# Performance work log

Hardware: AMD Instinct MI355X
Metric: run time of the kernel (lower is better)

Reference implementation:

```python
import jax, jax.numpy as jnp
import numpy as np

B, N = 4, 128
INPUT_SIZE, Z_SIZE = 512, 256
D_TENSOR, N_HEADS, SEQ_LEN = 64, 8, 64
D = D_TENSOR * N_HEADS * SEQ_LEN  # 32768


def setup_inputs() -> dict:
    key = jax.random.key(0)
    ks = jax.random.split(key, 10)
    s = lambda fan_in: 1.0 / np.sqrt(fan_in)
    return {
        "x": jax.random.normal(ks[0], (B, N, INPUT_SIZE), dtype=jnp.float32),
        "z": jax.random.normal(ks[1], (B, N, Z_SIZE), dtype=jnp.float32),
        "Wq": jax.random.uniform(ks[2], (Z_SIZE, D), jnp.float32, -s(Z_SIZE), s(Z_SIZE)),
        "bq": jax.random.uniform(ks[3], (D,), jnp.float32, -s(Z_SIZE), s(Z_SIZE)),
        "Wk": jax.random.uniform(ks[4], (INPUT_SIZE, D), jnp.float32, -s(INPUT_SIZE), s(INPUT_SIZE)),
        "bk": jax.random.uniform(ks[5], (D,), jnp.float32, -s(INPUT_SIZE), s(INPUT_SIZE)),
        "Wv": jax.random.uniform(ks[6], (INPUT_SIZE, D), jnp.float32, -s(INPUT_SIZE), s(INPUT_SIZE)),
        "bv": jax.random.uniform(ks[7], (D,), jnp.float32, -s(INPUT_SIZE), s(INPUT_SIZE)),
        "Wo": jax.random.uniform(ks[8], (D, INPUT_SIZE), jnp.float32, -s(D), s(D)),
        "bo": jax.random.uniform(ks[9], (INPUT_SIZE,), jnp.float32, -s(D), s(D)),
    }


def reference(x, z, Wq, bq, Wk, bk, Wv, bv, Wo, bo):
    # Q, K, V: [B, N, heads, seq_len, d_tensor]
    Q = (z @ Wq + bq).reshape(B, N, N_HEADS, SEQ_LEN, D_TENSOR)
    K = (x @ Wk + bk).reshape(B, N, N_HEADS, SEQ_LEN, D_TENSOR)
    V = (x @ Wv + bv).reshape(B, N, N_HEADS, SEQ_LEN, D_TENSOR)
    scores = jnp.einsum("bnhqd,bnhkd->bnhqk", Q, K) / np.sqrt(D_TENSOR).astype(np.float32)
    attn = jax.nn.softmax(scores, axis=-1)
    out = jnp.einsum("bnhqk,bnhkd->bnhqd", attn, V).reshape(B, N, D)
    return out @ Wo + bo
```

## Files before the change

### kernel.cpp

```cpp
#include <hip/hip_runtime.h>
#include <stdint.h>


typedef __attribute__((ext_vector_type(8))) short short8;
typedef __attribute__((ext_vector_type(4))) float floatx4;

__device__ __forceinline__ unsigned short f2bf(float f) {
  union { float f; unsigned int u; } v; v.f = f;
  unsigned int u = v.u + 0x7FFFu + ((v.u >> 16) & 1u);
  return (unsigned short)(u >> 16);
}

#define MFMA16(a, b, c) __builtin_amdgcn_mfma_f32_16x16x32_bf16((a), (b), (c), 0, 0, 0)

#define STAGE_TILE(SRC, LD, LDSARR)                                            \
  do {                                                                         \
    _Pragma("unroll") for (int i_ = 0; i_ < 4; ++i_) {                         \
      int e_ = tid + (i_ << 8);                                                \
      int r_ = e_ >> 3;                                                        \
      int c_ = (e_ & 7) ^ (r_ & 7);                                            \
      __builtin_amdgcn_global_load_lds(                                        \
          (const __attribute__((address_space(1))) unsigned int*)((SRC) +      \
              (size_t)r_ * (LD) + (c_ << 3)),                                  \
          (__attribute__((address_space(3))) unsigned int*)(&(LDSARR)[e_ << 3]),\
          16, 0, 0);                                                           \
    }                                                                          \
  } while (0)

#define FRAG(LDSARR, ROW, KS)                                                  \
  (*(const short8*)(&(LDSARR)[(((ROW) << 6)) +                                 \
      ((((((KS) << 2) + quad)) ^ ((ROW) & 7)) << 3)]))

__device__ __forceinline__ void transpose_body(const float* __restrict__ W,
                                               unsigned short* __restrict__ WT,
                                               int Kd, int Nd) {
  __shared__ __align__(16) float S[64 * 72];
  __shared__ __align__(16) unsigned short T[64 * 72];
  const int tid = threadIdx.x;
  const int n0 = blockIdx.x * 64, k0 = blockIdx.y * 64;
#pragma unroll
  for (int i = 0; i < 4; ++i) {
    int e = tid + (i << 8);
    int r = e >> 4, c = (e & 15) << 2;
    float4 w = *(const float4*)(W + (size_t)(k0 + r) * Nd + n0 + c);
    *(float4*)(&S[r * 72 + c]) = w;
  }
  __syncthreads();
  {
    const int n = tid & 63, kh = tid >> 6;
    float v[16];
#pragma unroll
    for (int j = 0; j < 16; ++j) v[j] = S[(kh * 16 + j) * 72 + n];
    uint4 p0, p1;
    p0.x = f2bf(v[0])  | ((unsigned)f2bf(v[1])  << 16);
    p0.y = f2bf(v[2])  | ((unsigned)f2bf(v[3])  << 16);
    p0.z = f2bf(v[4])  | ((unsigned)f2bf(v[5])  << 16);
    p0.w = f2bf(v[6])  | ((unsigned)f2bf(v[7])  << 16);
    p1.x = f2bf(v[8])  | ((unsigned)f2bf(v[9])  << 16);
    p1.y = f2bf(v[10]) | ((unsigned)f2bf(v[11]) << 16);
    p1.z = f2bf(v[12]) | ((unsigned)f2bf(v[13]) << 16);
    p1.w = f2bf(v[14]) | ((unsigned)f2bf(v[15]) << 16);
    *(uint4*)(&T[n * 72 + kh * 16])     = p0;
    *(uint4*)(&T[n * 72 + kh * 16 + 8]) = p1;
  }
  __syncthreads();
#pragma unroll
  for (int i = 0; i < 2; ++i) {
    int e = tid + (i << 8);
    int n = e >> 3, kc = e & 7;
    uint4 vv = *(const uint4*)(&T[n * 72 + kc * 8]);
    *(uint4*)(WT + (size_t)(n0 + n) * Kd + k0 + kc * 8) = vv;
  }
}

__global__ __launch_bounds__(256) void transpose_qkv(const float* __restrict__ Wq,
                                                     const float* __restrict__ Wk,
                                                     const float* __restrict__ Wv,
                                                     unsigned short* __restrict__ WqT,
                                                     unsigned short* __restrict__ WkT,
                                                     unsigned short* __restrict__ WvT,
                                                     const float* __restrict__ x,
                                                     const float* __restrict__ z,
                                                     unsigned short* __restrict__ xb,
                                                     unsigned short* __restrict__ zb) {
  const int zsel = blockIdx.z;
  if (zsel == 0) {
    if (blockIdx.y >= 4) return;
    transpose_body(Wq, WqT, 256, 32768);
  } else if (zsel == 1) {
    transpose_body(Wk, WkT, 512, 32768);
  } else if (zsel == 2) {
    transpose_body(Wv, WvT, 512, 32768);
  } else {
    if (blockIdx.y != 0 || blockIdx.x >= 192) return;
    int idx = (blockIdx.x * 256 + threadIdx.x) * 8;
    const float* src;
    unsigned short* dst;
    if (idx < 262144) { src = x + idx; dst = xb + idx; }
    else              { src = z + (idx - 262144); dst = zb + (idx - 262144); }
    float4 f0 = *(const float4*)src;
    float4 f1 = *(const float4*)(src + 4);
    uint4 p;
    p.x = f2bf(f0.x) | ((unsigned)f2bf(f0.y) << 16);
    p.y = f2bf(f0.z) | ((unsigned)f2bf(f0.w) << 16);
    p.z = f2bf(f1.x) | ((unsigned)f2bf(f1.y) << 16);
    p.w = f2bf(f1.z) | ((unsigned)f2bf(f1.w) << 16);
    *(uint4*)dst = p;
  }
}

__global__ __launch_bounds__(256) void transpose_wo(const float* __restrict__ W,
                                                    unsigned short* __restrict__ WT) {
  transpose_body(W, WT, 32768, 512);
}

__global__ __launch_bounds__(256) void gemm_qkv(const unsigned short* __restrict__ xb,
                                                const unsigned short* __restrict__ zb,
                                                const unsigned short* __restrict__ WqT,
                                                const unsigned short* __restrict__ WkT,
                                                const unsigned short* __restrict__ WvT,
                                                const float* __restrict__ bq,
                                                const float* __restrict__ bk,
                                                const float* __restrict__ bv,
                                                unsigned short* __restrict__ Qb,
                                                unsigned short* __restrict__ Kb,
                                                unsigned short* __restrict__ Vb) {
  __shared__ __align__(16) unsigned short As[128 * 64];
  __shared__ __align__(16) unsigned short Bs[128 * 64];
  const int tid = threadIdx.x;
  const int zsel = blockIdx.z;
  const unsigned short* A;
  const unsigned short* BT;
  const float* bias;
  unsigned short* C;
  int Ka;
  if (zsel == 0)      { A = zb; BT = WqT; bias = bq; C = Qb; Ka = 256; }
  else if (zsel == 1) { A = xb; BT = WkT; bias = bk; C = Kb; Ka = 512; }
  else                { A = xb; BT = WvT; bias = bv; C = Vb; Ka = 512; }
  const int lane = tid & 63, wid = tid >> 6;
  const int quad = lane >> 4, l15 = lane & 15;
  const int wm = wid >> 1, wn = wid & 1;
  const int m0 = blockIdx.y * 128, n0 = blockIdx.x * 128;
  floatx4 acc[4][4] = {};
  for (int k0 = 0; k0 < Ka; k0 += 64) {
    STAGE_TILE(A + (size_t)m0 * Ka + k0, Ka, As);
    STAGE_TILE(BT + (size_t)n0 * Ka + k0, Ka, Bs);
    __syncthreads();
#pragma unroll
    for (int ks = 0; ks < 2; ++ks) {
      short8 aF[4], bF[4];
#pragma unroll
      for (int mi = 0; mi < 4; ++mi) aF[mi] = FRAG(As, wm * 64 + mi * 16 + l15, ks);
#pragma unroll
      for (int ni = 0; ni < 4; ++ni) bF[ni] = FRAG(Bs, wn * 64 + ni * 16 + l15, ks);
#pragma unroll
      for (int mi = 0; mi < 4; ++mi)
#pragma unroll
        for (int ni = 0; ni < 4; ++ni)
          acc[mi][ni] = MFMA16(aF[mi], bF[ni], acc[mi][ni]);
    }
    __syncthreads();
  }
#pragma unroll
  for (int ni = 0; ni < 4; ++ni) {
    int col = n0 + wn * 64 + ni * 16 + l15;
    float bv2 = bias[col];
#pragma unroll
    for (int mi = 0; mi < 4; ++mi) {
      int row = m0 + wm * 64 + mi * 16 + (quad << 2);
#pragma unroll
      for (int r = 0; r < 4; ++r)
        C[(size_t)(row + r) * 32768 + col] = f2bf(acc[mi][ni][r] + bv2);
    }
  }
}

__global__ __launch_bounds__(256) void attn64(const unsigned short* __restrict__ Qb,
                                              const unsigned short* __restrict__ Kb,
                                              const unsigned short* __restrict__ Vb,
                                              unsigned short* __restrict__ Ob) {
  __shared__ __align__(16) unsigned short Qs[64 * 72];
  __shared__ __align__(16) unsigned short Ks[64 * 72];
  __shared__ __align__(16) unsigned short VT[64 * 72];
  __shared__ __align__(16) unsigned short Ps[64 * 72];
  const int tid = threadIdx.x;
  const int bn = blockIdx.x >> 3, h = blockIdx.x & 7;
  const size_t base = (size_t)bn * 32768 + (size_t)h * 4096;
  const unsigned short* q = Qb + base;
  const unsigned short* k = Kb + base;
  const unsigned short* v = Vb + base;
#pragma unroll
  for (int i = 0; i < 2; ++i) {
    int e = tid + (i << 8);
    int r = e >> 3, dblk = e & 7;
    *(uint4*)(&Qs[r * 72 + dblk * 8]) = *(const uint4*)(q + r * 64 + dblk * 8);
    *(uint4*)(&Ks[r * 72 + dblk * 8]) = *(const uint4*)(k + r * 64 + dblk * 8);
    uint4 vv = *(const uint4*)(v + r * 64 + dblk * 8);
    const unsigned short* pv = (const unsigned short*)&vv;
#pragma unroll
    for (int j = 0; j < 8; ++j)
      VT[(dblk * 8 + j) * 72 + r] = pv[j];
  }
  __syncthreads();
  const int lane = tid & 63, wid = tid >> 6;
  const int quad = lane >> 4, l15 = lane & 15;
  const int qs = wid << 4;
  short8 aq0 = *(const short8*)(&Qs[(qs + l15) * 72 + quad * 8]);
  short8 aq1 = *(const short8*)(&Qs[(qs + l15) * 72 + 32 + quad * 8]);
  floatx4 s[4] = {};
#pragma unroll
  for (int ni = 0; ni < 4; ++ni) {
    short8 b0 = *(const short8*)(&Ks[(ni * 16 + l15) * 72 + quad * 8]);
    short8 b1 = *(const short8*)(&Ks[(ni * 16 + l15) * 72 + 32 + quad * 8]);
    s[ni] = MFMA16(aq0, b0, s[ni]);
    s[ni] = MFMA16(aq1, b1, s[ni]);
  }
#pragma unroll
  for (int r = 0; r < 4; ++r) {
    float e0 = s[0][r] * 0.125f, e1 = s[1][r] * 0.125f;
    float e2 = s[2][r] * 0.125f, e3 = s[3][r] * 0.125f;
    float m = fmaxf(fmaxf(e0, e1), fmaxf(e2, e3));
    m = fmaxf(m, __shfl_xor(m, 1));
    m = fmaxf(m, __shfl_xor(m, 2));
    m = fmaxf(m, __shfl_xor(m, 4));
    m = fmaxf(m, __shfl_xor(m, 8));
    float x0 = __expf(e0 - m), x1 = __expf(e1 - m);
    float x2 = __expf(e2 - m), x3 = __expf(e3 - m);
    float t = x0 + x1 + x2 + x3;
    t += __shfl_xor(t, 1); t += __shfl_xor(t, 2);
    t += __shfl_xor(t, 4); t += __shfl_xor(t, 8);
    float inv = __builtin_amdgcn_rcpf(t);
    int row = qs + (quad << 2) + r;
    Ps[row * 72 +      l15] = f2bf(x0 * inv);
    Ps[row * 72 + 16 + l15] = f2bf(x1 * inv);
    Ps[row * 72 + 32 + l15] = f2bf(x2 * inv);
    Ps[row * 72 + 48 + l15] = f2bf(x3 * inv);
  }
  __syncthreads();
  short8 ap0 = *(const short8*)(&Ps[(qs + l15) * 72 + quad * 8]);
  short8 ap1 = *(const short8*)(&Ps[(qs + l15) * 72 + 32 + quad * 8]);
  floatx4 o[4] = {};
#pragma unroll
  for (int ni = 0; ni < 4; ++ni) {
    short8 b0 = *(const short8*)(&VT[(ni * 16 + l15) * 72 + quad * 8]);
    short8 b1 = *(const short8*)(&VT[(ni * 16 + l15) * 72 + 32 + quad * 8]);
    o[ni] = MFMA16(ap0, b0, o[ni]);
    o[ni] = MFMA16(ap1, b1, o[ni]);
  }
  unsigned short* outp = Ob + base;
#pragma unroll
  for (int ni = 0; ni < 4; ++ni)
#pragma unroll
    for (int r = 0; r < 4; ++r)
      outp[(qs + (quad << 2) + r) * 64 + ni * 16 + l15] = f2bf(o[ni][r]);
}

__global__ __launch_bounds__(256) void gemm_out(const unsigned short* __restrict__ A,
                                                const unsigned short* __restrict__ BT,
                                                const float* __restrict__ bias,
                                                float* __restrict__ C) {
  __shared__ __align__(16) unsigned short As[128 * 64];
  __shared__ __align__(16) unsigned short Bs[128 * 64];
  const int tid = threadIdx.x;
  const int lane = tid & 63, wid = tid >> 6;
  const int quad = lane >> 4, l15 = lane & 15;
  const int wm = wid >> 1, wn = wid & 1;
  const int m0 = blockIdx.y * 128, n0 = blockIdx.x * 128;
  const int kbase = blockIdx.z * 1024;
  floatx4 acc[4][4] = {};
  for (int k0 = kbase; k0 < kbase + 1024; k0 += 64) {
    STAGE_TILE(A + (size_t)m0 * 32768 + k0, 32768, As);
    STAGE_TILE(BT + (size_t)n0 * 32768 + k0, 32768, Bs);
    __syncthreads();
#pragma unroll
    for (int ks = 0; ks < 2; ++ks) {
      short8 aF[4], bF[4];
#pragma unroll
      for (int mi = 0; mi < 4; ++mi) aF[mi] = FRAG(As, wm * 64 + mi * 16 + l15, ks);
#pragma unroll
      for (int ni = 0; ni < 4; ++ni) bF[ni] = FRAG(Bs, wn * 64 + ni * 16 + l15, ks);
#pragma unroll
      for (int mi = 0; mi < 4; ++mi)
#pragma unroll
        for (int ni = 0; ni < 4; ++ni)
          acc[mi][ni] = MFMA16(aF[mi], bF[ni], acc[mi][ni]);
    }
    __syncthreads();
  }
#pragma unroll
  for (int ni = 0; ni < 4; ++ni) {
    int col = n0 + wn * 64 + ni * 16 + l15;
    float bv = (blockIdx.z == 0) ? bias[col] : 0.0f;
#pragma unroll
    for (int mi = 0; mi < 4; ++mi) {
      int row = m0 + wm * 64 + mi * 16 + (quad << 2);
#pragma unroll
      for (int r = 0; r < 4; ++r)
        atomicAdd(&C[(size_t)(row + r) * 512 + col], acc[mi][ni][r] + bv);
    }
  }
}

extern "C" void kernel_launch(void* const* d_in, const int* in_sizes, int n_in,
                              void* d_out, int out_size, void* d_ws, size_t ws_size,
                              hipStream_t stream) {
  const float* x  = (const float*)d_in[0];
  const float* z  = (const float*)d_in[1];
  const float* Wq = (const float*)d_in[2];
  const float* bq = (const float*)d_in[3];
  const float* Wk = (const float*)d_in[4];
  const float* bk = (const float*)d_in[5];
  const float* Wv = (const float*)d_in[6];
  const float* bv = (const float*)d_in[7];
  const float* Wo = (const float*)d_in[8];
  const float* bo = (const float*)d_in[9];
  float* out = (float*)d_out;
  char* ws = (char*)d_ws;

  unsigned short* WqT = (unsigned short*)(ws + 0);
  unsigned short* WkT = (unsigned short*)(ws + 16777216);
  unsigned short* WvT = (unsigned short*)(ws + 50331648);
  unsigned short* Qb  = (unsigned short*)(ws + 83886080);
  unsigned short* Kb  = (unsigned short*)(ws + 117440512);
  unsigned short* Vb  = (unsigned short*)(ws + 150994944);
  unsigned short* Ob  = (unsigned short*)(ws + 0);
  unsigned short* WoT = (unsigned short*)(ws + 50331648);

  unsigned short* xb = (unsigned short*)d_out;
  unsigned short* zb = (unsigned short*)((char*)d_out + 524288);

  transpose_qkv<<<dim3(512, 8, 4), 256, 0, stream>>>(Wq, Wk, Wv, WqT, WkT, WvT,
                                                     x, z, xb, zb);

  gemm_qkv<<<dim3(256, 4, 3), 256, 0, stream>>>(xb, zb, WqT, WkT, WvT,
                                                bq, bk, bv, Qb, Kb, Vb);

  transpose_wo<<<dim3(8, 512), 256, 0, stream>>>(Wo, WoT);

  attn64<<<dim3(4096), 256, 0, stream>>>(Qb, Kb, Vb, Ob);

  hipMemsetAsync(d_out, 0, (size_t)out_size * sizeof(float), stream);
  gemm_out<<<dim3(4, 4, 32), 256, 0, stream>>>(Ob, WoT, bo, out);
}
```

Baseline: 384.3 us.

## Widen QKV GEMM tile to 128x256 and loop transposes over column strips

The QKV projection GEMM now computes a 128x256 output tile per block, with twice the B staging and an 8-wide accumulator array per warp, so each A tile is reused across more columns and fewer blocks are launched. The weight transpose kernels now process eight 64-column sub-tiles per block in a loop, which cuts the grid size by 8x, and the x/z conversion indexing is remapped to fit the smaller grid. The aim is less redundant A-tile traffic and lower block scheduling overhead. In exchange the GEMM uses more registers and LDS per block, which may lower occupancy, and the transposes have less parallelism per launch (transpose_wo drops to 512 blocks).

```diff
diff --git a/kernel.cpp b/kernel.cpp
--- a/kernel.cpp
+++ b/kernel.cpp
@@ -13,9 +13,9 @@
 
 #define MFMA16(a, b, c) __builtin_amdgcn_mfma_f32_16x16x32_bf16((a), (b), (c), 0, 0, 0)
 
-#define STAGE_TILE(SRC, LD, LDSARR)                                            \
+#define STAGE_ROWS(SRC, LD, LDSARR, NIT)                                       \
   do {                                                                         \
-    _Pragma("unroll") for (int i_ = 0; i_ < 4; ++i_) {                         \
+    _Pragma("unroll") for (int i_ = 0; i_ < (NIT); ++i_) {                     \
       int e_ = tid + (i_ << 8);                                                \
       int r_ = e_ >> 3;                                                        \
       int c_ = (e_ & 7) ^ (r_ & 7);                                            \
@@ -31,45 +31,49 @@
   (*(const short8*)(&(LDSARR)[(((ROW) << 6)) +                                 \
       ((((((KS) << 2) + quad)) ^ ((ROW) & 7)) << 3)]))
 
-__device__ __forceinline__ void transpose_body(const float* __restrict__ W,
-                                               unsigned short* __restrict__ WT,
-                                               int Kd, int Nd) {
+__device__ __forceinline__ void transpose_strip(const float* __restrict__ W,
+                                                unsigned short* __restrict__ WT,
+                                                int Kd, int Nd) {
   __shared__ __align__(16) float S[64 * 72];
   __shared__ __align__(16) unsigned short T[64 * 72];
   const int tid = threadIdx.x;
-  const int n0 = blockIdx.x * 64, k0 = blockIdx.y * 64;
-#pragma unroll
-  for (int i = 0; i < 4; ++i) {
-    int e = tid + (i << 8);
-    int r = e >> 4, c = (e & 15) << 2;
-    float4 w = *(const float4*)(W + (size_t)(k0 + r) * Nd + n0 + c);
-    *(float4*)(&S[r * 72 + c]) = w;
-  }
-  __syncthreads();
-  {
-    const int n = tid & 63, kh = tid >> 6;
-    float v[16];
-#pragma unroll
-    for (int j = 0; j < 16; ++j) v[j] = S[(kh * 16 + j) * 72 + n];
-    uint4 p0, p1;
-    p0.x = f2bf(v[0])  | ((unsigned)f2bf(v[1])  << 16);
-    p0.y = f2bf(v[2])  | ((unsigned)f2bf(v[3])  << 16);
-    p0.z = f2bf(v[4])  | ((unsigned)f2bf(v[5])  << 16);
-    p0.w = f2bf(v[6])  | ((unsigned)f2bf(v[7])  << 16);
-    p1.x = f2bf(v[8])  | ((unsigned)f2bf(v[9])  << 16);
-    p1.y = f2bf(v[10]) | ((unsigned)f2bf(v[11]) << 16);
-    p1.z = f2bf(v[12]) | ((unsigned)f2bf(v[13]) << 16);
-    p1.w = f2bf(v[14]) | ((unsigned)f2bf(v[15]) << 16);
-    *(uint4*)(&T[n * 72 + kh * 16])     = p0;
-    *(uint4*)(&T[n * 72 + kh * 16 + 8]) = p1;
-  }
-  __syncthreads();
-#pragma unroll
-  for (int i = 0; i < 2; ++i) {
-    int e = tid + (i << 8);
-    int n = e >> 3, kc = e & 7;
-    uint4 vv = *(const uint4*)(&T[n * 72 + kc * 8]);
-    *(uint4*)(WT + (size_t)(n0 + n) * Kd + k0 + kc * 8) = vv;
+  const int k0 = blockIdx.y * 64;
+  int n0 = blockIdx.x * 512;
+#pragma unroll 1
+  for (int sub = 0; sub < 8; ++sub, n0 += 64) {
+#pragma unroll
+    for (int i = 0; i < 4; ++i) {
+      int e = tid + (i << 8);
+      int r = e >> 4, c = (e & 15) << 2;
+      float4 w = *(const float4*)(W + (size_t)(k0 + r) * Nd + n0 + c);
+      *(float4*)(&S[r * 72 + c]) = w;
+    }
+    __syncthreads();
+    {
+      const int n = tid & 63, kh = tid >> 6;
+      float v[16];
+#pragma unroll
+      for (int j = 0; j < 16; ++j) v[j] = S[(kh * 16 + j) * 72 + n];
+      uint4 p0, p1;
+      p0.x = f2bf(v[0])  | ((unsigned)f2bf(v[1])  << 16);
+      p0.y = f2bf(v[2])  | ((unsigned)f2bf(v[3])  << 16);
+      p0.z = f2bf(v[4])  | ((unsigned)f2bf(v[5])  << 16);
+      p0.w = f2bf(v[6])  | ((unsigned)f2bf(v[7])  << 16);
+      p1.x = f2bf(v[8])  | ((unsigned)f2bf(v[9])  << 16);
+      p1.y = f2bf(v[10]) | ((unsigned)f2bf(v[11]) << 16);
+      p1.z = f2bf(v[12]) | ((unsigned)f2bf(v[13]) << 16);
+      p1.w = f2bf(v[14]) | ((unsigned)f2bf(v[15]) << 16);
+      *(uint4*)(&T[n * 72 + kh * 16])     = p0;
+      *(uint4*)(&T[n * 72 + kh * 16 + 8]) = p1;
+    }
+    __syncthreads();
+#pragma unroll
+    for (int i = 0; i < 2; ++i) {
+      int e = tid + (i << 8);
+      int n = e >> 3, kc = e & 7;
+      uint4 vv = *(const uint4*)(&T[n * 72 + kc * 8]);
+      *(uint4*)(WT + (size_t)(n0 + n) * Kd + k0 + kc * 8) = vv;
+    }
   }
 }
 
@@ -86,14 +90,15 @@
   const int zsel = blockIdx.z;
   if (zsel == 0) {
     if (blockIdx.y >= 4) return;
-    transpose_body(Wq, WqT, 256, 32768);
+    transpose_strip(Wq, WqT, 256, 32768);
   } else if (zsel == 1) {
-    transpose_body(Wk, WkT, 512, 32768);
+    transpose_strip(Wk, WkT, 512, 32768);
   } else if (zsel == 2) {
-    transpose_body(Wv, WvT, 512, 32768);
+    transpose_strip(Wv, WvT, 512, 32768);
   } else {
-    if (blockIdx.y != 0 || blockIdx.x >= 192) return;
-    int idx = (blockIdx.x * 256 + threadIdx.x) * 8;
+    int fb = blockIdx.y * 64 + blockIdx.x;
+    if (fb >= 192) return;
+    int idx = (fb * 256 + threadIdx.x) * 8;
     const float* src;
     unsigned short* dst;
     if (idx < 262144) { src = x + idx; dst = xb + idx; }
@@ -111,7 +116,7 @@
 
 __global__ __launch_bounds__(256) void transpose_wo(const float* __restrict__ W,
                                                     unsigned short* __restrict__ WT) {
-  transpose_body(W, WT, 32768, 512);
+  transpose_strip(W, WT, 32768, 512);
 }
 
 __global__ __launch_bounds__(256) void gemm_qkv(const unsigned short* __restrict__ xb,
@@ -126,7 +131,7 @@
                                                 unsigned short* __restrict__ Kb,
                                                 unsigned short* __restrict__ Vb) {
   __shared__ __align__(16) unsigned short As[128 * 64];
-  __shared__ __align__(16) unsigned short Bs[128 * 64];
+  __shared__ __align__(16) unsigned short Bs[256 * 64];
   const int tid = threadIdx.x;
   const int zsel = blockIdx.z;
   const unsigned short* A;
@@ -140,30 +145,30 @@
   const int lane = tid & 63, wid = tid >> 6;
   const int quad = lane >> 4, l15 = lane & 15;
   const int wm = wid >> 1, wn = wid & 1;
-  const int m0 = blockIdx.y * 128, n0 = blockIdx.x * 128;
-  floatx4 acc[4][4] = {};
+  const int m0 = blockIdx.y * 128, n0 = blockIdx.x * 256;
+  floatx4 acc[4][8] = {};
   for (int k0 = 0; k0 < Ka; k0 += 64) {
-    STAGE_TILE(A + (size_t)m0 * Ka + k0, Ka, As);
-    STAGE_TILE(BT + (size_t)n0 * Ka + k0, Ka, Bs);
+    STAGE_ROWS(A + (size_t)m0 * Ka + k0, Ka, As, 4);
+    STAGE_ROWS(BT + (size_t)n0 * Ka + k0, Ka, Bs, 8);
     __syncthreads();
 #pragma unroll
     for (int ks = 0; ks < 2; ++ks) {
-      short8 aF[4], bF[4];
+      short8 aF[4], bF[8];
 #pragma unroll
       for (int mi = 0; mi < 4; ++mi) aF[mi] = FRAG(As, wm * 64 + mi * 16 + l15, ks);
 #pragma unroll
-      for (int ni = 0; ni < 4; ++ni) bF[ni] = FRAG(Bs, wn * 64 + ni * 16 + l15, ks);
+      for (int ni = 0; ni < 8; ++ni) bF[ni] = FRAG(Bs, wn * 128 + ni * 16 + l15, ks);
 #pragma unroll
       for (int mi = 0; mi < 4; ++mi)
 #pragma unroll
-        for (int ni = 0; ni < 4; ++ni)
+        for (int ni = 0; ni < 8; ++ni)
           acc[mi][ni] = MFMA16(aF[mi], bF[ni], acc[mi][ni]);
     }
     __syncthreads();
   }
 #pragma unroll
-  for (int ni = 0; ni < 4; ++ni) {
-    int col = n0 + wn * 64 + ni * 16 + l15;
+  for (int ni = 0; ni < 8; ++ni) {
+    int col = n0 + wn * 128 + ni * 16 + l15;
     float bv2 = bias[col];
 #pragma unroll
     for (int mi = 0; mi < 4; ++mi) {
@@ -269,8 +274,8 @@
   const int kbase = blockIdx.z * 1024;
   floatx4 acc[4][4] = {};
   for (int k0 = kbase; k0 < kbase + 1024; k0 += 64) {
-    STAGE_TILE(A + (size_t)m0 * 32768 + k0, 32768, As);
-    STAGE_TILE(BT + (size_t)n0 * 32768 + k0, 32768, Bs);
+    STAGE_ROWS(A + (size_t)m0 * 32768 + k0, 32768, As, 4);
+    STAGE_ROWS(BT + (size_t)n0 * 32768 + k0, 32768, Bs, 4);
     __syncthreads();
 #pragma unroll
     for (int ks = 0; ks < 2; ++ks) {
@@ -329,13 +334,13 @@
   unsigned short* xb = (unsigned short*)d_out;
   unsigned short* zb = (unsigned short*)((char*)d_out + 524288);
 
-  transpose_qkv<<<dim3(512, 8, 4), 256, 0, stream>>>(Wq, Wk, Wv, WqT, WkT, WvT,
-                                                     x, z, xb, zb);
-
-  gemm_qkv<<<dim3(256, 4, 3), 256, 0, stream>>>(xb, zb, WqT, WkT, WvT,
+  transpose_qkv<<<dim3(64, 8, 4), 256, 0, stream>>>(Wq, Wk, Wv, WqT, WkT, WvT,
+                                                    x, z, xb, zb);
+
+  gemm_qkv<<<dim3(128, 4, 3), 256, 0, stream>>>(xb, zb, WqT, WkT, WvT,
                                                 bq, bk, bv, Qb, Kb, Vb);
 
-  transpose_wo<<<dim3(8, 512), 256, 0, stream>>>(Wo, WoT);
+  transpose_wo<<<dim3(1, 512), 256, 0, stream>>>(Wo, WoT);
 
   attn64<<<dim3(4096), 256, 0, stream>>>(Qb, Kb, Vb, Ob);
 
```

After: 420.3 us. 9.4% more time.
